# Optimization experiments

Measured on AMD Instinct MI355X. Metric: run time of the kernel, lower is better.

Reference implementation:

```python
import jax, jax.numpy as jnp
import numpy as np

B, C, H, W = 16, 256, 96, 96
CQ = C // 8      # 32, query/key channels in CrossAttention
CM = C // 2      # 128, inter_planes


def conv1x1(x, w, b=None):
    # x: [B,Cin,H,W], w: [Cout,Cin]
    y = jnp.einsum('bchw,oc->bohw', x, w)
    if b is not None:
        y = y + b[None, :, None, None]
    return y


def cross_attention(x, wq, bq, wk, bk, wv, bv, gamma):
    # criss-cross (axial H and W) attention with -inf diagonal on the H branch
    b_, c_, h_, w_ = x.shape
    q = conv1x1(x, wq, bq)  # [B,CQ,H,W]
    k = conv1x1(x, wk, bk)
    v = conv1x1(x, wv, bv)  # [B,C,H,W]
    # energy over column (H axis): [B,H,W,H], masked diag h==h'
    e_h = jnp.einsum('bchw,bckw->bhwk', q, k)
    diag = jnp.eye(h_, dtype=bool)[None, :, None, :]  # [1,H,1,H]
    e_h = jnp.where(diag, -jnp.inf, e_h)
    # energy over row (W axis): [B,H,W,W]
    e_w = jnp.einsum('bchw,bchv->bhwv', q, k)
    att = jax.nn.softmax(jnp.concatenate([e_h, e_w], axis=3), axis=3)
    a_h, a_w = att[..., :h_], att[..., h_:]
    out_h = jnp.einsum('bckw,bhwk->bchw', v, a_h)
    out_w = jnp.einsum('bchv,bhwv->bchw', v, a_w)
    return gamma * (out_h + out_w) + x


def spatial_weighted(x, w_q_right, w_v_right, w_up, b_up):
    b_, _, h_, w_ = x.shape
    inp = conv1x1(x, w_v_right).reshape(b_, CM, h_ * w_)        # [B,CM,HW]
    mask = conv1x1(x, w_q_right).reshape(b_, 1, h_ * w_)        # [B,1,HW]
    mask = jax.nn.softmax(mask, axis=2)
    ctx = jnp.einsum('bcn,bon->bco', inp, mask)                 # [B,CM,1]
    ctx = jnp.einsum('bci,oc->boi', ctx, w_up) + b_up[None, :, None]  # [B,C,1]
    mask_ch = jax.nn.sigmoid(ctx)[..., None]                    # [B,C,1,1]
    return x * mask_ch


def channel_weighted(x, w_q_left, w_v_left):
    b_, _, h_, w_ = x.shape
    g = conv1x1(x, w_q_left)                                    # [B,CM,H,W]
    avg = jnp.mean(g, axis=(2, 3))                              # [B,CM]
    theta = conv1x1(x, w_v_left).reshape(b_, CM, h_ * w_)       # [B,CM,HW]
    ctx = jnp.einsum('bc,bcn->bn', avg, theta)                  # [B,HW]
    ctx = jax.nn.softmax(ctx, axis=1).reshape(b_, 1, h_, w_)
    return x * jax.nn.sigmoid(ctx)


def setup_inputs() -> dict:
    key = jax.random.key(0)
    ks = jax.random.split(key, 16)
    s = lambda fan_in: (2.0 / fan_in) ** 0.5
    inp = {
        'x': jax.random.normal(ks[0], (B, C, H, W), jnp.float32),
        'w_q_right': jax.random.normal(ks[1], (1, C), jnp.float32) * s(C),
        'w_v_right': jax.random.normal(ks[2], (CM, C), jnp.float32) * s(C),
        'w_up': jax.random.normal(ks[3], (C, CM), jnp.float32) * s(CM),
        'b_up': jnp.zeros((C,), jnp.float32),
        'w_q_left': jax.random.normal(ks[4], (CM, C), jnp.float32) * s(C),
        'w_v_left': jax.random.normal(ks[5], (CM, C), jnp.float32) * s(C),
        'cr_wq': jax.random.normal(ks[6], (CQ, C), jnp.float32) * s(C),
        'cr_bq': jnp.zeros((CQ,), jnp.float32),
        'cr_wk': jax.random.normal(ks[7], (CQ, C), jnp.float32) * s(C),
        'cr_bk': jnp.zeros((CQ,), jnp.float32),
        'cr_wv': jax.random.normal(ks[8], (C, C), jnp.float32) * s(C),
        'cr_bv': jnp.zeros((C,), jnp.float32),
        'gamma': jax.random.normal(ks[9], (1,), jnp.float32) * 0.1,
    }
    return inp


def reference(x, w_q_right, w_v_right, w_up, b_up, w_q_left, w_v_left,
              cr_wq, cr_bq, cr_wk, cr_bk, cr_wv, cr_bv, gamma):
    cross = lambda t: cross_attention(t, cr_wq, cr_bq, cr_wk, cr_bk, cr_wv, cr_bv, gamma)
    ctx_channel = cross(spatial_weighted(x, w_q_right, w_v_right, w_up, b_up))
    ctx_spatial = cross(channel_weighted(x, w_q_left, w_v_left))
    return cross(ctx_spatial + ctx_channel)
```

## Files before the change

### kernel.cpp

```cpp
#include <hip/hip_runtime.h>
#include <math.h>

#define Bn 16
#define Cn 256
#define Hn 96
#define Wn 96
#define Nn 9216
#define PIXn 147456
#define XSZk ((size_t)Bn*Cn*Nn)
#define YSZk ((size_t)Bn*64*Nn)
#define ATTSZ ((size_t)PIXn*96)

typedef short bf8 __attribute__((ext_vector_type(8)));
typedef float f32x4 __attribute__((ext_vector_type(4)));
#define MFMA(a,b,c) __builtin_amdgcn_mfma_f32_16x16x32_bf16(a,b,c,0,0,0)

typedef unsigned short ushort_t;
typedef _Float16 h16;

__device__ inline ushort_t f2bf(float f){
  union{float f; unsigned int u;} v; v.f=f;
  unsigned int r = v.u + 0x7fffu + ((v.u>>16)&1u);
  return (ushort_t)(r>>16);
}
__device__ inline float bf2f(ushort_t s){
  union{unsigned int u; float f;} v; v.u = ((unsigned int)s)<<16;
  return v.f;
}
__device__ inline ushort_t f2h(float f){
  union{h16 h; ushort_t u;} v; v.h=(h16)f; return v.u;
}
__device__ inline float h2f(ushort_t u){
  union{ushort_t u; h16 h;} v; v.u=u; return (float)v.h;
}

__device__ inline float waveSum(float v){
#pragma unroll
  for(int o=32;o;o>>=1) v += __shfl_down(v,o,64);
  return v;
}
__device__ inline float waveMax(float v){
#pragma unroll
  for(int o=32;o;o>>=1) v = fmaxf(v,__shfl_down(v,o,64));
  return v;
}


__global__ __launch_bounds__(1024) void k_pass1(const float* __restrict__ x,
    const float* __restrict__ wqr, float* __restrict__ xmean,
    float* __restrict__ partp){
  int cg = blockIdx.x, b = blockIdx.y, tid = threadIdx.x;
  __shared__ float r16[16];
  float mp[9];
#pragma unroll
  for(int k=0;k<9;k++) mp[k]=0.f;
  for(int cc=0;cc<16;cc++){
    int c = cg*16+cc;
    const float* row = x + ((size_t)b*Cn + c)*Nn;
    float w = wqr[c];
    float s = 0.f;
#pragma unroll
    for(int k=0;k<9;k++){
      float v = row[k*1024+tid];
      s += v;
      mp[k] += w*v;
    }
    s = waveSum(s);
    if((tid&63)==0) r16[tid>>6]=s;
    __syncthreads();
    if(tid==0){
      float t=0.f;
      for(int i=0;i<16;i++) t+=r16[i];
      xmean[(size_t)b*Cn + c] = t*(1.f/Nn);
    }
    __syncthreads();
  }
  float* dst = partp + ((size_t)cg*Bn + b)*Nn;
#pragma unroll
  for(int k=0;k<9;k++) dst[k*1024+tid]=mp[k];
}

__global__ __launch_bounds__(1024) void k_pass2(const float* __restrict__ x,
    const float* __restrict__ wvec, const float* __restrict__ maskb,
    float* __restrict__ xw, float* __restrict__ partp){
  int cg = blockIdx.x, b = blockIdx.y, tid = threadIdx.x;
  __shared__ float r16[16];
  float cp[9], mk[9];
#pragma unroll
  for(int k=0;k<9;k++){
    cp[k]=0.f;
    mk[k]=maskb[(size_t)b*Nn + k*1024+tid];
  }
  for(int cc=0;cc<16;cc++){
    int c = cg*16+cc;
    const float* row = x + ((size_t)b*Cn + c)*Nn;
    float w = wvec[(size_t)b*Cn + c];
    float s = 0.f;
#pragma unroll
    for(int k=0;k<9;k++){
      float v = row[k*1024+tid];
      s += mk[k]*v;
      cp[k] += w*v;
    }
    s = waveSum(s);
    if((tid&63)==0) r16[tid>>6]=s;
    __syncthreads();
    if(tid==0){
      float t=0.f;
      for(int i=0;i<16;i++) t+=r16[i];
      xw[(size_t)b*Cn + c] = t;
    }
    __syncthreads();
  }
  float* dst = partp + ((size_t)cg*Bn + b)*Nn;
#pragma unroll
  for(int k=0;k<9;k++) dst[k*1024+tid]=cp[k];
}

__global__ void k_red16(const float* __restrict__ part, float* __restrict__ out){
  size_t p = (size_t)blockIdx.x*256 + threadIdx.x;
  float s=0.f;
#pragma unroll
  for(int cg=0;cg<16;cg++) s += part[(size_t)cg*Bn*Nn + p];
  out[p]=s;
}

__global__ void k_small1(const float* __restrict__ xmean, const float* __restrict__ wql,
                         const float* __restrict__ wvl, float* __restrict__ wvec){
  int b=blockIdx.x, t=threadIdx.x;
  __shared__ float xm[Cn];
  __shared__ float av[128];
  xm[t] = xmean[b*Cn+t];
  __syncthreads();
  if(t<128){
    float s=0.f;
    for(int c=0;c<Cn;c++) s += wql[t*Cn+c]*xm[c];
    av[t]=s;
  }
  __syncthreads();
  float s=0.f;
  for(int m=0;m<128;m++) s += av[m]*wvl[m*Cn+t];
  wvec[b*Cn+t]=s;
}

__global__ void k_softmax_n(const float* __restrict__ in, float* __restrict__ out, int mode){
  int b=blockIdx.x, tid=threadIdx.x, lane=tid&63, wid=tid>>6;
  const float* p = in + (size_t)b*Nn;
  __shared__ float red[16];
  __shared__ float bc2[2];
  float mx=-3e38f;
  for(int i=tid;i<Nn;i+=1024) mx=fmaxf(mx,p[i]);
  mx = waveMax(mx);
  if(lane==0) red[wid]=mx;
  __syncthreads();
  if(tid==0){ float m=red[0]; for(int i=1;i<16;i++) m=fmaxf(m,red[i]); bc2[0]=m; }
  __syncthreads();
  mx=bc2[0];
  float s=0.f;
  for(int i=tid;i<Nn;i+=1024) s+=expf(p[i]-mx);
  s = waveSum(s);
  __syncthreads();
  if(lane==0) red[wid]=s;
  __syncthreads();
  if(tid==0){ float t=0.f; for(int i=0;i<16;i++) t+=red[i]; bc2[1]=t; }
  __syncthreads();
  float inv=1.f/bc2[1];
  for(int i=tid;i<Nn;i+=1024){
    float e=expf(p[i]-mx)*inv;
    out[(size_t)b*Nn+i] = mode ? 1.f/(1.f+expf(-e)) : e;
  }
}

__global__ void k_small2(const float* __restrict__ xw, const float* __restrict__ wvr,
                         const float* __restrict__ wup, const float* __restrict__ bup,
                         float* __restrict__ g1){
  int b=blockIdx.x, t=threadIdx.x;
  __shared__ float xs[Cn];
  __shared__ float cx[128];
  xs[t]=xw[b*Cn+t];
  __syncthreads();
  if(t<128){
    float s=0.f;
    for(int c=0;c<Cn;c++) s += wvr[t*Cn+c]*xs[c];
    cx[t]=s;
  }
  __syncthreads();
  float s=bup[t];
  for(int m=0;m<128;m++) s += wup[t*128+m]*cx[m];
  g1[b*Cn+t]=1.f/(1.f+expf(-s));
}


__global__ void k_packb(const float* __restrict__ wq, const float* __restrict__ bq,
                        const float* __restrict__ wk, const float* __restrict__ bk,
                        const float* __restrict__ wv, const float* __restrict__ bv,
                        ushort_t* __restrict__ Wp, float* __restrict__ bp){
  int o = blockIdx.x, t = threadIdx.x;
  const float* src; float bs;
  if(o<32){ src = wq + o*Cn; bs = bq[o]; }
  else if(o<64){ src = wk + (o-32)*Cn; bs = bk[o-32]; }
  else { src = wv + (o-64)*Cn; bs = bv[o-64]; }
  Wp[o*Cn+t] = f2bf(src[t]);
  if(t==0) bp[o] = bs;
}

#define AP 40
#define BP 264
#define GP 68

template<int GATED>
__global__ __launch_bounds__(256) void k_gemm_qkv(
    const ushort_t* __restrict__ tb, const float* __restrict__ x,
    const float* __restrict__ g1, const float* __restrict__ m2,
    const ushort_t* __restrict__ Wp, const float* __restrict__ bp,
    ushort_t* __restrict__ Yqk, ushort_t* __restrict__ Vb, int selbase){
  __shared__ ushort_t SM[320*AP + 64*BP];
  __shared__ float gsh[256];
  ushort_t* Ws = SM;
  ushort_t* Bt = SM + 320*AP;
  int by = blockIdx.y, b = by & 15, sl = by >> 4;
  int sel = selbase + sl;
  int n0 = blockIdx.x*64;
  int tid = threadIdx.x, lane = tid&63, wid = tid>>6;

  if(GATED){
    gsh[tid] = g1[b*Cn + tid];
    __syncthreads();
    const float* xb = x + (size_t)b*Cn*Nn + n0 + (tid&63);
    float scl_n = (sel==1) ? m2[(size_t)b*Nn + n0 + (tid&63)] : 0.f;
    int cg = (tid>>6)*8;
#pragma unroll
    for(int p=0;p<8;p++){
      int c8 = p*32 + cg;
      float fv[8];
#pragma unroll
      for(int k2=0;k2<8;k2++){
        float xf = xb[(size_t)(c8+k2)*Nn];
        fv[k2] = xf * (sel==0 ? gsh[c8+k2] : scl_n);
      }
      uint4 pk;
      pk.x = (unsigned)f2bf(fv[0]) | ((unsigned)f2bf(fv[1])<<16);
      pk.y = (unsigned)f2bf(fv[2]) | ((unsigned)f2bf(fv[3])<<16);
      pk.z = (unsigned)f2bf(fv[4]) | ((unsigned)f2bf(fv[5])<<16);
      pk.w = (unsigned)f2bf(fv[6]) | ((unsigned)f2bf(fv[7])<<16);
      *(uint4*)&Bt[(tid&63)*BP + c8] = pk;
    }
  } else {
    const ushort_t* xb = tb + (size_t)b*Cn*Nn + n0 + (tid&63);
    int cg = (tid>>6)*8;
#pragma unroll
    for(int p=0;p<8;p++){
      int c8 = p*32 + cg;
      unsigned e0=xb[(size_t)(c8+0)*Nn], e1=xb[(size_t)(c8+1)*Nn];
      unsigned e2=xb[(size_t)(c8+2)*Nn], e3=xb[(size_t)(c8+3)*Nn];
      unsigned e4=xb[(size_t)(c8+4)*Nn], e5=xb[(size_t)(c8+5)*Nn];
      unsigned e6=xb[(size_t)(c8+6)*Nn], e7=xb[(size_t)(c8+7)*Nn];
      uint4 pk;
      pk.x = e0 | (e1<<16); pk.y = e2 | (e3<<16);
      pk.z = e4 | (e5<<16); pk.w = e6 | (e7<<16);
      *(uint4*)&Bt[(tid&63)*BP + c8] = pk;
    }
  }

  f32x4 acc[5][4];
#pragma unroll
  for(int f=0;f<5;f++)
#pragma unroll
    for(int g=0;g<4;g++) acc[f][g] = (f32x4){0.f,0.f,0.f,0.f};

  for(int ki=0;ki<8;ki++){
    __syncthreads();
#pragma unroll
    for(int q=0;q<5;q++){
      int fidx = q*256 + tid;
      int o = fidx>>2, kk = (fidx&3)*8;
      uint4 wv = *(const uint4*)&Wp[o*Cn + ki*32 + kk];
      *(uint4*)&Ws[o*AP + kk] = wv;
    }
    __syncthreads();
    bf8 bfr[4];
#pragma unroll
    for(int g=0;g<4;g++)
      bfr[g] = *(const bf8*)&Bt[(g*16 + (lane&15))*BP + ki*32 + (lane>>4)*8];
#pragma unroll
    for(int f=0;f<5;f++){
      bf8 a = *(const bf8*)&Ws[(wid*80 + f*16 + (lane&15))*AP + (lane>>4)*8];
#pragma unroll
      for(int g=0;g<4;g++) acc[f][g] = MFMA(a, bfr[g], acc[f][g]);
    }
  }

  __syncthreads();
#pragma unroll
  for(int f=0;f<5;f++){
    int o = wid*80 + f*16 + (lane>>4)*4;
#pragma unroll
    for(int i=0;i<4;i++){
      float bias = bp[o+i];
#pragma unroll
      for(int g=0;g<4;g++)
        SM[(o+i)*GP + g*16 + (lane&15)] = f2bf(acc[f][g][i] + bias);
    }
  }
  __syncthreads();
  ushort_t* Yo = Yqk + (size_t)sl*YSZk;
  ushort_t* Vo = Vb  + (size_t)sl*XSZk;
  for(int u=tid; u<320*8; u+=256){
    int lo_ = u>>3, c8 = (u&7)*8;
    ushort_t* dst = (lo_<64) ? (Yo + ((size_t)b*64 + lo_)*Nn)
                             : (Vo + ((size_t)b*Cn + (lo_-64))*Nn);
    *(uint4*)&dst[n0 + c8] = *(uint4*)&SM[lo_*GP + c8];
  }
}

__global__ __launch_bounds__(256) void k_transpose_b(const ushort_t* __restrict__ src,
                                                     ushort_t* __restrict__ dst){
  __shared__ ushort_t Ls[96*98];
  size_t base = (size_t)blockIdx.x * Nn;
  int tid = threadIdx.x;
  for(int e=tid*2; e<Nn; e+=512){
    unsigned int u = *(const unsigned int*)&src[base+e];
    int r=e/96, c=e%96;
    *(unsigned int*)&Ls[r*98+c] = u;
  }
  __syncthreads();
  for(int e=tid*2; e<Nn; e+=512){
    int r=e/96, c=e%96;
    unsigned int u = (unsigned int)Ls[c*98+r] | (((unsigned int)Ls[(c+1)*98+r])<<16);
    *(unsigned int*)&dst[base+e] = u;
  }
}

__global__ __launch_bounds__(256) void k_e2(const ushort_t* __restrict__ Yqk,
    const ushort_t* __restrict__ Yqkt, ushort_t* __restrict__ attl,
    ushort_t* __restrict__ attr){
  __shared__ ushort_t Qt[96*AP];
  __shared__ ushort_t Kt[96*AP];
  int r = blockIdx.x, mode = blockIdx.y;
  int zz = blockIdx.z, b = zz & 15, sl = zz >> 4;
  const ushort_t* Y = (mode ? Yqk : Yqkt) + (size_t)sl*YSZk;
  int pm   = mode ? 1  : 96;
  int pr   = mode ? 96 : 1;
  ushort_t* attx = (mode ? attr : attl) + (size_t)sl*ATTSZ;
  int tid = threadIdx.x, lane = tid&63, wid = tid>>6;
  {
    int half = tid>>7;
    int cg   = (tid>>5)&3;
    int l32  = tid&31;
    ushort_t* T = half ? Kt : Qt;
    const ushort_t* S = Y + ((size_t)b*64 + half*32 + cg*8)*Nn + (size_t)r*96;
#pragma unroll
    for(int p=0;p<3;p++){
      int sp = p*32 + l32;
      unsigned e0=S[(size_t)0*Nn+sp], e1=S[(size_t)1*Nn+sp];
      unsigned e2=S[(size_t)2*Nn+sp], e3=S[(size_t)3*Nn+sp];
      unsigned e4=S[(size_t)4*Nn+sp], e5=S[(size_t)5*Nn+sp];
      unsigned e6=S[(size_t)6*Nn+sp], e7=S[(size_t)7*Nn+sp];
      uint4 pk;
      pk.x = e0 | (e1<<16); pk.y = e2 | (e3<<16);
      pk.z = e4 | (e5<<16); pk.w = e6 | (e7<<16);
      *(uint4*)&T[sp*AP + cg*8] = pk;
    }
  }
  __syncthreads();
  int mb = (wid>>1)*48, nb = (wid&1)*48;
  const f32x4 z4 = {0.f,0.f,0.f,0.f};
  f32x4 acc[3][3];
  bf8 a[3], bb[3];
#pragma unroll
  for(int f=0;f<3;f++) a[f] = *(const bf8*)&Qt[(mb+f*16+(lane&15))*AP + (lane>>4)*8];
#pragma unroll
  for(int g=0;g<3;g++) bb[g] = *(const bf8*)&Kt[(nb+g*16+(lane&15))*AP + (lane>>4)*8];
#pragma unroll
  for(int f=0;f<3;f++)
#pragma unroll
    for(int g=0;g<3;g++) acc[f][g] = MFMA(a[f], bb[g], z4);
#pragma unroll
  for(int f=0;f<3;f++)
#pragma unroll
    for(int i=0;i<4;i++){
      int m = mb + f*16 + (lane>>4)*4 + i;
      ushort_t* arow = attx + ((size_t)b*Nn + (size_t)m*pm + (size_t)r*pr)*96;
#pragma unroll
      for(int g=0;g<3;g++){
        int n = nb + g*16 + (lane&15);
        arow[n] = f2h(acc[f][g][i]);
      }
    }
}

__global__ __launch_bounds__(256) void k_softmax_ip(ushort_t* attl, ushort_t* attr){
  int wave = threadIdx.x>>6, l = threadIdx.x&63;
  int t = blockIdx.x*4 + wave;
  int zz = blockIdx.z, b = zz & 15, sl = zz >> 4;
  attl += (size_t)sl*ATTSZ; attr += (size_t)sl*ATTSZ;
  int i=0, base=0;
  while(base + (96-i) <= t){ base += 96-i; i++; }
  int j = i + (t-base);
  int hf = l>>5, l32 = l&31;
  int h = hf ? j : i, w = hf ? i : j;
  size_t p = (size_t)b*Nn + (size_t)h*96 + w;
  const ushort_t* al = attl + p*96;
  const ushort_t* ar = attr + p*96;
  float v[6];
#pragma unroll
  for(int k=0;k<3;k++){
    int el = l32 + 32*k;
    float vv = h2f(al[el]);
    v[k] = (el==h) ? -1e30f : vv;
  }
#pragma unroll
  for(int k=0;k<3;k++) v[3+k] = h2f(ar[l32 + 32*k]);
  float mx = v[0];
#pragma unroll
  for(int k=1;k<6;k++) mx = fmaxf(mx, v[k]);
#pragma unroll
  for(int o=16;o;o>>=1) mx = fmaxf(mx, __shfl_xor(mx, o, 64));
  float e[6], s=0.f;
#pragma unroll
  for(int k=0;k<6;k++){ e[k]=expf(v[k]-mx); s+=e[k]; }
#pragma unroll
  for(int o=16;o;o>>=1) s += __shfl_xor(s, o, 64);
  float inv = 1.f/s;
  size_t q = (size_t)b*Nn + (size_t)w*96 + h;
  ushort_t* oh = attl + q*96;
  ushort_t* ow = attr + p*96;
#pragma unroll
  for(int k=0;k<3;k++) oh[l32+32*k] = f2bf(e[k]*inv);
#pragma unroll
  for(int k=0;k<3;k++) ow[l32+32*k] = f2bf(e[3+k]*inv);
}

#define SP 120
#define RP 100

template<int FIN>
__global__ __launch_bounds__(256) void k_pv2(const ushort_t* __restrict__ VB,
    const ushort_t* __restrict__ VTb, const ushort_t* __restrict__ attw,
    const ushort_t* __restrict__ atth, const float* __restrict__ x,
    const float* __restrict__ g1, const float* __restrict__ m2,
    const ushort_t* __restrict__ residb, ushort_t* TT, float* __restrict__ Of,
    ushort_t* OTb, const float* __restrict__ gp, int selbase){
  __shared__ ushort_t SMEM[128*RP];
  int r = blockIdx.x, mode = blockIdx.y>>1, half = blockIdx.y&1;
  int zz = blockIdx.z, b = zz & 15, sl = zz >> 4;
  int sel = selbase + sl;
  float gm = gp[0];
  int tid = threadIdx.x, lane = tid&63, wid = tid>>6;
  const ushort_t* V = (mode ? VTb : VB) + (size_t)sl*XSZk;
  size_t vbase = (size_t)b*Cn*Nn + (size_t)r*96;
  bf8 vf[6];
#pragma unroll
  for(int f=0;f<2;f++)
#pragma unroll
    for(int j=0;j<3;j++)
      vf[f*3+j] = *(const bf8*)&V[vbase
        + (size_t)(half*128 + wid*32 + f*16 + (lane&15))*Nn + j*32 + (lane>>4)*8];
  const ushort_t* ab = (mode ? atth : attw) + (size_t)sl*ATTSZ
                     + ((size_t)b*Nn + (size_t)r*96)*96;
  for(int u=tid; u<96*12; u+=256){
    int n=u/12, j8=(u%12)*8;
    uint4 q = *(const uint4*)&ab[n*96 + j8];
    *(uint4*)&SMEM[n*SP + j8] = q;
  }
  __syncthreads();
  f32x4 acc[2][6];
#pragma unroll
  for(int f=0;f<2;f++)
#pragma unroll
    for(int g=0;g<6;g++) acc[f][g] = (f32x4){0.f,0.f,0.f,0.f};
#pragma unroll
  for(int j0=0;j0<3;j0++){
    bf8 bfr[6];
#pragma unroll
    for(int g=0;g<6;g++)
      bfr[g] = *(const bf8*)&SMEM[(g*16+(lane&15))*SP + j0*32 + (lane>>4)*8];
#pragma unroll
    for(int f=0;f<2;f++)
#pragma unroll
      for(int g=0;g<6;g++) acc[f][g] = MFMA(vf[f*3+j0], bfr[g], acc[f][g]);
  }
  __syncthreads();
#pragma unroll
  for(int f=0;f<2;f++){
    int lr = wid*32 + f*16 + (lane>>4)*4;
#pragma unroll
    for(int i=0;i<4;i++)
#pragma unroll
      for(int g=0;g<6;g++)
        SMEM[(lr+i)*RP + g*16 + (lane&15)] = f2bf(gm*acc[f][g][i]);
  }
  __syncthreads();
  ushort_t* OT = OTb + (size_t)sl*XSZk;
  ushort_t* To = TT + (size_t)sel*XSZk;
  for(int u=tid; u<128*12; u+=256){
    int lc = u/12, q8 = (u%12)*8;
    int c = half*128 + lc;
    size_t row = vbase + (size_t)c*Nn;
    uint4 v = *(uint4*)&SMEM[lc*RP + q8];
    if(mode){
      *(uint4*)&OT[row + q8] = v;
    } else {
      unsigned* vp=(unsigned*)&v;
      if(FIN){
        uint4 rv = *(const uint4*)&residb[row + q8];
        unsigned* rp=(unsigned*)&rv;
        float4 o1, o2;
        o1.x = bf2f((ushort_t)(vp[0]&0xffff)) + bf2f((ushort_t)(rp[0]&0xffff));
        o1.y = bf2f((ushort_t)(vp[0]>>16))    + bf2f((ushort_t)(rp[0]>>16));
        o1.z = bf2f((ushort_t)(vp[1]&0xffff)) + bf2f((ushort_t)(rp[1]&0xffff));
        o1.w = bf2f((ushort_t)(vp[1]>>16))    + bf2f((ushort_t)(rp[1]>>16));
        o2.x = bf2f((ushort_t)(vp[2]&0xffff)) + bf2f((ushort_t)(rp[2]&0xffff));
        o2.y = bf2f((ushort_t)(vp[2]>>16))    + bf2f((ushort_t)(rp[2]>>16));
        o2.z = bf2f((ushort_t)(vp[3]&0xffff)) + bf2f((ushort_t)(rp[3]&0xffff));
        o2.w = bf2f((ushort_t)(vp[3]>>16))    + bf2f((ushort_t)(rp[3]>>16));
        *(float4*)&Of[row + q8]     = o1;
        *(float4*)&Of[row + q8 + 4] = o2;
      } else {
        float4 x1 = *(const float4*)&x[row + q8];
        float4 x2 = *(const float4*)&x[row + q8 + 4];
        float rs[8];
        if(sel==0){
          float g = g1[b*Cn + c];
          rs[0]=x1.x*g; rs[1]=x1.y*g; rs[2]=x1.z*g; rs[3]=x1.w*g;
          rs[4]=x2.x*g; rs[5]=x2.y*g; rs[6]=x2.z*g; rs[7]=x2.w*g;
        } else {
          float4 m1 = *(const float4*)&m2[(size_t)b*Nn + (size_t)r*96 + q8];
          float4 m2v= *(const float4*)&m2[(size_t)b*Nn + (size_t)r*96 + q8 + 4];
          rs[0]=x1.x*m1.x; rs[1]=x1.y*m1.y; rs[2]=x1.z*m1.z; rs[3]=x1.w*m1.w;
          rs[4]=x2.x*m2v.x; rs[5]=x2.y*m2v.y; rs[6]=x2.z*m2v.z; rs[7]=x2.w*m2v.w;
        }
        uint4 o; unsigned* op=(unsigned*)&o;
#pragma unroll
        for(int k=0;k<4;k++){
          float lo = bf2f((ushort_t)(vp[k]&0xffff)) + rs[2*k];
          float hi = bf2f((ushort_t)(vp[k]>>16))    + rs[2*k+1];
          op[k] = (unsigned)f2bf(lo) | ((unsigned)f2bf(hi)<<16);
        }
        *(uint4*)&To[row + q8] = o;
      }
    }
  }
}

template<int VAR>
__global__ __launch_bounds__(256) void k_merge(float* __restrict__ outf,
    ushort_t* __restrict__ outb, const ushort_t* __restrict__ add,
    const ushort_t* __restrict__ OT){
  __shared__ ushort_t Ls[96*98];
  __shared__ ushort_t Ls2[(VAR==3)?96*98:1];
  size_t base = (size_t)blockIdx.x * Nn;
  int tid = threadIdx.x;
  for(int e=tid*2; e<Nn; e+=512){
    int r=e/96, c=e%96;
    *(unsigned int*)&Ls[r*98+c] = *(const unsigned int*)&OT[base+e];
    if(VAR==3)
      *(unsigned int*)&Ls2[r*98+c] = *(const unsigned int*)&OT[XSZk + base + e];
  }
  __syncthreads();
  for(int e=tid*4; e<Nn; e+=1024){
    int r=e/96, c=e%96;
    float t0 = bf2f(Ls[(c+0)*98+r]), t1 = bf2f(Ls[(c+1)*98+r]);
    float t2 = bf2f(Ls[(c+2)*98+r]), t3 = bf2f(Ls[(c+3)*98+r]);
    if(VAR==3){
      t0 += bf2f(Ls2[(c+0)*98+r]); t1 += bf2f(Ls2[(c+1)*98+r]);
      t2 += bf2f(Ls2[(c+2)*98+r]); t3 += bf2f(Ls2[(c+3)*98+r]);
    }
    if(VAR==1){
      float4 o = *(float4*)&outf[base+e];
      o.x += t0; o.y += t1; o.z += t2; o.w += t3;
      *(float4*)&outf[base+e] = o;
    } else {
      uint2 u = *(uint2*)&outb[base+e];
      float a0 = bf2f((ushort_t)(u.x&0xffff)) + t0;
      float a1 = bf2f((ushort_t)(u.x>>16))    + t1;
      float a2 = bf2f((ushort_t)(u.y&0xffff)) + t2;
      float a3 = bf2f((ushort_t)(u.y>>16))    + t3;
      if(VAR==2 || VAR==3){
        uint2 v = *(const uint2*)&add[base+e];
        a0 += bf2f((ushort_t)(v.x&0xffff));
        a1 += bf2f((ushort_t)(v.x>>16));
        a2 += bf2f((ushort_t)(v.y&0xffff));
        a3 += bf2f((ushort_t)(v.y>>16));
      }
      u.x = (unsigned)f2bf(a0) | ((unsigned)f2bf(a1)<<16);
      u.y = (unsigned)f2bf(a2) | ((unsigned)f2bf(a3)<<16);
      *(uint2*)&outb[base+e] = u;
    }
  }
}

extern "C" void kernel_launch(void* const* d_in, const int* in_sizes, int n_in,
                              void* d_out, int out_size, void* d_ws, size_t ws_size,
                              hipStream_t stream){
  const float* x    = (const float*)d_in[0];
  const float* wqr  = (const float*)d_in[1];
  const float* wvr  = (const float*)d_in[2];
  const float* wup  = (const float*)d_in[3];
  const float* bup  = (const float*)d_in[4];
  const float* wql  = (const float*)d_in[5];
  const float* wvl  = (const float*)d_in[6];
  const float* crwq = (const float*)d_in[7];
  const float* crbq = (const float*)d_in[8];
  const float* crwk = (const float*)d_in[9];
  const float* crbk = (const float*)d_in[10];
  const float* crwv = (const float*)d_in[11];
  const float* crbv = (const float*)d_in[12];
  const float* gma  = (const float*)d_in[13];
  float* out = (float*)d_out;

  const int nsel = (ws_size >= (size_t)654000000) ? 2 : 1;

  char* wsb = (char*)d_ws;
  ushort_t* TT   = (ushort_t*)wsb; wsb += 2*XSZk*2;
  ushort_t* VB2  = (ushort_t*)wsb; wsb += (size_t)nsel*XSZk*2;
  ushort_t* VT2  = (ushort_t*)wsb; wsb += (size_t)nsel*XSZk*2;
  ushort_t* Y2   = (ushort_t*)wsb; wsb += (size_t)nsel*YSZk*2;
  ushort_t* Yt2  = (ushort_t*)wsb; wsb += (size_t)nsel*YSZk*2;
  ushort_t* ATTL = (ushort_t*)wsb; wsb += (size_t)nsel*ATTSZ*2;
  ushort_t* ATTR = (ushort_t*)wsb; wsb += (size_t)nsel*ATTSZ*2;
  float*    partp= (float*)wsb;    wsb += (size_t)16*Bn*Nn*4;
  ushort_t* Wpb  = (ushort_t*)wsb; wsb += 320*Cn*2;
  float*    bp   = (float*)wsb;    wsb += 320*4;
  float*    xmean= (float*)wsb;    wsb += Bn*Cn*4;
  float*    wvec = (float*)wsb;    wsb += Bn*Cn*4;
  float*    xw   = (float*)wsb;    wsb += Bn*Cn*4;
  float*    g1   = (float*)wsb;    wsb += Bn*Cn*4;
  float*    mraw = (float*)wsb;    wsb += (size_t)PIXn*4;
  float*    maskb= (float*)wsb;    wsb += (size_t)PIXn*4;
  float*    craw = (float*)wsb;    wsb += (size_t)PIXn*4;
  float*    m2   = (float*)wsb;    wsb += (size_t)PIXn*4;

  k_packb<<<320,256,0,stream>>>(crwq,crbq,crwk,crbk,crwv,crbv,Wpb,bp);

  k_pass1<<<dim3(16,Bn),1024,0,stream>>>(x, wqr, xmean, partp);
  k_red16<<<Bn*Nn/256,256,0,stream>>>(partp, mraw);
  k_small1<<<Bn,256,0,stream>>>(xmean, wql, wvl, wvec);
  k_softmax_n<<<Bn,1024,0,stream>>>(mraw, maskb, 0);
  k_pass2<<<dim3(16,Bn),1024,0,stream>>>(x, wvec, maskb, xw, partp);
  k_red16<<<Bn*Nn/256,256,0,stream>>>(partp, craw);
  k_softmax_n<<<Bn,1024,0,stream>>>(craw, m2, 1);
  k_small2<<<Bn,256,0,stream>>>(xw, wvr, wup, bup, g1);

  auto cross12 = [&](int selbase, int nsl){
    k_gemm_qkv<1><<<dim3(Nn/64,Bn*nsl),256,0,stream>>>(nullptr, x, g1, m2, Wpb, bp, Y2, VB2, selbase);
    k_transpose_b<<<Bn*64*nsl,256,0,stream>>>(Y2, Yt2);
    k_e2<<<dim3(96,2,Bn*nsl),256,0,stream>>>(Y2, Yt2, ATTL, ATTR);
    k_softmax_ip<<<dim3(1164,1,Bn*nsl),256,0,stream>>>(ATTL, ATTR);
    k_transpose_b<<<Bn*Cn*nsl,256,0,stream>>>(VB2, VT2);
    k_pv2<0><<<dim3(96,4,Bn*nsl),256,0,stream>>>(VB2, VT2, ATTR, ATTL,
        x, g1, m2, nullptr, TT, nullptr, VT2, gma, selbase);
  };

  ushort_t* T2p = TT + XSZk;
  if(nsel==2){
    cross12(0, 2);
    k_merge<3><<<Bn*Cn,256,0,stream>>>(nullptr, TT, T2p, VT2);
  } else {
    cross12(0, 1);
    k_merge<0><<<Bn*Cn,256,0,stream>>>(nullptr, TT, nullptr, VT2);
    cross12(1, 1);
    k_merge<2><<<Bn*Cn,256,0,stream>>>(nullptr, TT, T2p, VT2);
  }

  k_gemm_qkv<0><<<dim3(Nn/64,Bn),256,0,stream>>>(TT, nullptr, nullptr, nullptr, Wpb, bp, Y2, VB2, 0);
  k_transpose_b<<<Bn*64,256,0,stream>>>(Y2, Yt2);
  k_e2<<<dim3(96,2,Bn),256,0,stream>>>(Y2, Yt2, ATTL, ATTR);
  k_softmax_ip<<<dim3(1164,1,Bn),256,0,stream>>>(ATTL, ATTR);
  k_transpose_b<<<Bn*Cn,256,0,stream>>>(VB2, VT2);
  k_pv2<1><<<dim3(96,4,Bn),256,0,stream>>>(VB2, VT2, ATTR, ATTL,
      nullptr, nullptr, nullptr, TT, nullptr, out, VT2, gma, 0);
  k_merge<1><<<Bn*Cn,256,0,stream>>>(out, nullptr, nullptr, VT2);
}
```

Measured before the change: 1.145 ms.

## Cache bf16 copy of x, vectorize reductions, drop batched dual-branch path

The first reduction pass now also writes a bf16 copy of x into the workspace. Later passes (pass2, the gated QKV GEMM and the PV residual) read this half-size copy instead of fp32 x when the workspace is large enough. The pass kernels switch to float4-vectorized contiguous chunks of 8 pixels per thread. The two-slice batched cross-attention path is removed in favour of always running the branches sequentially. The final PV now writes a bf16 intermediate that a new merge variant adds into the fp32 output. This cuts fp32 read traffic but adds extra rounding of x and loses the batched-branch concurrency.

```diff
diff --git a/kernel.cpp b/kernel.cpp
--- a/kernel.cpp
+++ b/kernel.cpp
@@ -46,24 +46,41 @@
 }
 
 
+template<int XBW>
 __global__ __launch_bounds__(1024) void k_pass1(const float* __restrict__ x,
     const float* __restrict__ wqr, float* __restrict__ xmean,
-    float* __restrict__ partp){
+    float* __restrict__ partp, ushort_t* __restrict__ XB){
   int cg = blockIdx.x, b = blockIdx.y, tid = threadIdx.x;
   __shared__ float r16[16];
-  float mp[9];
-#pragma unroll
-  for(int k=0;k<9;k++) mp[k]=0.f;
+  float mp[2][8];
+#pragma unroll
+  for(int u=0;u<2;u++)
+#pragma unroll
+    for(int e=0;e<8;e++) mp[u][e]=0.f;
   for(int cc=0;cc<16;cc++){
     int c = cg*16+cc;
     const float* row = x + ((size_t)b*Cn + c)*Nn;
     float w = wqr[c];
     float s = 0.f;
 #pragma unroll
-    for(int k=0;k<9;k++){
-      float v = row[k*1024+tid];
-      s += v;
-      mp[k] += w*v;
+    for(int u=0;u<2;u++){
+      int ch = tid + u*1024;
+      if(ch < 1152){
+        float4 a = *(const float4*)&row[ch*8];
+        float4 d = *(const float4*)&row[ch*8+4];
+        float v0=a.x,v1=a.y,v2=a.z,v3=a.w,v4=d.x,v5=d.y,v6=d.z,v7=d.w;
+        s += ((v0+v1)+(v2+v3))+((v4+v5)+(v6+v7));
+        mp[u][0]+=w*v0; mp[u][1]+=w*v1; mp[u][2]+=w*v2; mp[u][3]+=w*v3;
+        mp[u][4]+=w*v4; mp[u][5]+=w*v5; mp[u][6]+=w*v6; mp[u][7]+=w*v7;
+        if(XBW){
+          uint4 pk;
+          pk.x=(unsigned)f2bf(v0)|((unsigned)f2bf(v1)<<16);
+          pk.y=(unsigned)f2bf(v2)|((unsigned)f2bf(v3)<<16);
+          pk.z=(unsigned)f2bf(v4)|((unsigned)f2bf(v5)<<16);
+          pk.w=(unsigned)f2bf(v6)|((unsigned)f2bf(v7)<<16);
+          *(uint4*)&XB[((size_t)b*Cn + c)*Nn + ch*8] = pk;
+        }
+      }
     }
     s = waveSum(s);
     if((tid&63)==0) r16[tid>>6]=s;
@@ -77,30 +94,68 @@
   }
   float* dst = partp + ((size_t)cg*Bn + b)*Nn;
 #pragma unroll
-  for(int k=0;k<9;k++) dst[k*1024+tid]=mp[k];
-}
-
+  for(int u=0;u<2;u++){
+    int ch = tid + u*1024;
+    if(ch < 1152){
+      float4 o1, o2;
+      o1.x=mp[u][0]; o1.y=mp[u][1]; o1.z=mp[u][2]; o1.w=mp[u][3];
+      o2.x=mp[u][4]; o2.y=mp[u][5]; o2.z=mp[u][6]; o2.w=mp[u][7];
+      *(float4*)&dst[ch*8]   = o1;
+      *(float4*)&dst[ch*8+4] = o2;
+    }
+  }
+}
+
+template<int XBR>
 __global__ __launch_bounds__(1024) void k_pass2(const float* __restrict__ x,
-    const float* __restrict__ wvec, const float* __restrict__ maskb,
-    float* __restrict__ xw, float* __restrict__ partp){
+    const ushort_t* __restrict__ XB, const float* __restrict__ wvec,
+    const float* __restrict__ maskb, float* __restrict__ xw,
+    float* __restrict__ partp){
   int cg = blockIdx.x, b = blockIdx.y, tid = threadIdx.x;
   __shared__ float r16[16];
-  float cp[9], mk[9];
-#pragma unroll
-  for(int k=0;k<9;k++){
-    cp[k]=0.f;
-    mk[k]=maskb[(size_t)b*Nn + k*1024+tid];
+  float cp[2][8], mk[2][8];
+#pragma unroll
+  for(int u=0;u<2;u++){
+    int ch = tid + u*1024;
+    if(ch < 1152){
+      float4 a = *(const float4*)&maskb[(size_t)b*Nn + ch*8];
+      float4 d = *(const float4*)&maskb[(size_t)b*Nn + ch*8 + 4];
+      mk[u][0]=a.x; mk[u][1]=a.y; mk[u][2]=a.z; mk[u][3]=a.w;
+      mk[u][4]=d.x; mk[u][5]=d.y; mk[u][6]=d.z; mk[u][7]=d.w;
+    }
+#pragma unroll
+    for(int e=0;e<8;e++) cp[u][e]=0.f;
   }
   for(int cc=0;cc<16;cc++){
     int c = cg*16+cc;
-    const float* row = x + ((size_t)b*Cn + c)*Nn;
     float w = wvec[(size_t)b*Cn + c];
     float s = 0.f;
 #pragma unroll
-    for(int k=0;k<9;k++){
-      float v = row[k*1024+tid];
-      s += mk[k]*v;
-      cp[k] += w*v;
+    for(int u=0;u<2;u++){
+      int ch = tid + u*1024;
+      if(ch < 1152){
+        float v[8];
+        if(XBR){
+          uint4 q = *(const uint4*)&XB[((size_t)b*Cn + c)*Nn + ch*8];
+          unsigned* qp=(unsigned*)&q;
+#pragma unroll
+          for(int k=0;k<4;k++){
+            v[2*k]   = bf2f((ushort_t)(qp[k]&0xffff));
+            v[2*k+1] = bf2f((ushort_t)(qp[k]>>16));
+          }
+        } else {
+          const float* row = x + ((size_t)b*Cn + c)*Nn;
+          float4 a = *(const float4*)&row[ch*8];
+          float4 d = *(const float4*)&row[ch*8+4];
+          v[0]=a.x; v[1]=a.y; v[2]=a.z; v[3]=a.w;
+          v[4]=d.x; v[5]=d.y; v[6]=d.z; v[7]=d.w;
+        }
+#pragma unroll
+        for(int e=0;e<8;e++){
+          s += mk[u][e]*v[e];
+          cp[u][e] += w*v[e];
+        }
+      }
     }
     s = waveSum(s);
     if((tid&63)==0) r16[tid>>6]=s;
@@ -114,7 +169,16 @@
   }
   float* dst = partp + ((size_t)cg*Bn + b)*Nn;
 #pragma unroll
-  for(int k=0;k<9;k++) dst[k*1024+tid]=cp[k];
+  for(int u=0;u<2;u++){
+    int ch = tid + u*1024;
+    if(ch < 1152){
+      float4 o1, o2;
+      o1.x=cp[u][0]; o1.y=cp[u][1]; o1.z=cp[u][2]; o1.w=cp[u][3];
+      o2.x=cp[u][4]; o2.y=cp[u][5]; o2.z=cp[u][6]; o2.w=cp[u][7];
+      *(float4*)&dst[ch*8]   = o1;
+      *(float4*)&dst[ch*8+4] = o2;
+    }
+  }
 }
 
 __global__ void k_red16(const float* __restrict__ part, float* __restrict__ out){
@@ -208,35 +272,44 @@
 #define BP 264
 #define GP 68
 
-template<int GATED>
+template<int GATED, int XBR>
 __global__ __launch_bounds__(256) void k_gemm_qkv(
     const ushort_t* __restrict__ tb, const float* __restrict__ x,
+    const ushort_t* __restrict__ XBp,
     const float* __restrict__ g1, const float* __restrict__ m2,
     const ushort_t* __restrict__ Wp, const float* __restrict__ bp,
-    ushort_t* __restrict__ Yqk, ushort_t* __restrict__ Vb, int selbase){
+    ushort_t* __restrict__ Yqk, ushort_t* __restrict__ Vb, int sel){
   __shared__ ushort_t SM[320*AP + 64*BP];
   __shared__ float gsh[256];
   ushort_t* Ws = SM;
   ushort_t* Bt = SM + 320*AP;
-  int by = blockIdx.y, b = by & 15, sl = by >> 4;
-  int sel = selbase + sl;
+  int b = blockIdx.y;
   int n0 = blockIdx.x*64;
   int tid = threadIdx.x, lane = tid&63, wid = tid>>6;
 
   if(GATED){
     gsh[tid] = g1[b*Cn + tid];
     __syncthreads();
-    const float* xb = x + (size_t)b*Cn*Nn + n0 + (tid&63);
     float scl_n = (sel==1) ? m2[(size_t)b*Nn + n0 + (tid&63)] : 0.f;
     int cg = (tid>>6)*8;
 #pragma unroll
     for(int p=0;p<8;p++){
       int c8 = p*32 + cg;
       float fv[8];
-#pragma unroll
-      for(int k2=0;k2<8;k2++){
-        float xf = xb[(size_t)(c8+k2)*Nn];
-        fv[k2] = xf * (sel==0 ? gsh[c8+k2] : scl_n);
+      if(XBR){
+        const ushort_t* xb = XBp + (size_t)b*Cn*Nn + n0 + (tid&63);
+#pragma unroll
+        for(int k2=0;k2<8;k2++){
+          float xf = bf2f(xb[(size_t)(c8+k2)*Nn]);
+          fv[k2] = xf * (sel==0 ? gsh[c8+k2] : scl_n);
+        }
+      } else {
+        const float* xb = x + (size_t)b*Cn*Nn + n0 + (tid&63);
+#pragma unroll
+        for(int k2=0;k2<8;k2++){
+          float xf = xb[(size_t)(c8+k2)*Nn];
+          fv[k2] = xf * (sel==0 ? gsh[c8+k2] : scl_n);
+        }
       }
       uint4 pk;
       pk.x = (unsigned)f2bf(fv[0]) | ((unsigned)f2bf(fv[1])<<16);
@@ -303,12 +376,10 @@
     }
   }
   __syncthreads();
-  ushort_t* Yo = Yqk + (size_t)sl*YSZk;
-  ushort_t* Vo = Vb  + (size_t)sl*XSZk;
   for(int u=tid; u<320*8; u+=256){
     int lo_ = u>>3, c8 = (u&7)*8;
-    ushort_t* dst = (lo_<64) ? (Yo + ((size_t)b*64 + lo_)*Nn)
-                             : (Vo + ((size_t)b*Cn + (lo_-64))*Nn);
+    ushort_t* dst = (lo_<64) ? (Yqk + ((size_t)b*64 + lo_)*Nn)
+                             : (Vb + ((size_t)b*Cn + (lo_-64))*Nn);
     *(uint4*)&dst[n0 + c8] = *(uint4*)&SM[lo_*GP + c8];
   }
 }
@@ -336,12 +407,11 @@
     ushort_t* __restrict__ attr){
   __shared__ ushort_t Qt[96*AP];
   __shared__ ushort_t Kt[96*AP];
-  int r = blockIdx.x, mode = blockIdx.y;
-  int zz = blockIdx.z, b = zz & 15, sl = zz >> 4;
-  const ushort_t* Y = (mode ? Yqk : Yqkt) + (size_t)sl*YSZk;
+  int r = blockIdx.x, mode = blockIdx.y, b = blockIdx.z;
+  const ushort_t* Y = mode ? Yqk : Yqkt;
   int pm   = mode ? 1  : 96;
   int pr   = mode ? 96 : 1;
-  ushort_t* attx = (mode ? attr : attl) + (size_t)sl*ATTSZ;
+  ushort_t* attx = mode ? attr : attl;
   int tid = threadIdx.x, lane = tid&63, wid = tid>>6;
   {
     int half = tid>>7;
@@ -392,8 +462,7 @@
 __global__ __launch_bounds__(256) void k_softmax_ip(ushort_t* attl, ushort_t* attr){
   int wave = threadIdx.x>>6, l = threadIdx.x&63;
   int t = blockIdx.x*4 + wave;
-  int zz = blockIdx.z, b = zz & 15, sl = zz >> 4;
-  attl += (size_t)sl*ATTSZ; attr += (size_t)sl*ATTSZ;
+  int b = blockIdx.z;
   int i=0, base=0;
   while(base + (96-i) <= t){ base += 96-i; i++; }
   int j = i + (t-base);
@@ -434,20 +503,19 @@
 #define SP 120
 #define RP 100
 
-template<int FIN>
+template<int RES, int XBR>
 __global__ __launch_bounds__(256) void k_pv2(const ushort_t* __restrict__ VB,
     const ushort_t* __restrict__ VTb, const ushort_t* __restrict__ attw,
     const ushort_t* __restrict__ atth, const float* __restrict__ x,
+    const ushort_t* __restrict__ XBp,
     const float* __restrict__ g1, const float* __restrict__ m2,
-    const ushort_t* __restrict__ residb, ushort_t* TT, float* __restrict__ Of,
-    ushort_t* OTb, const float* __restrict__ gp, int selbase){
+    const ushort_t* __restrict__ residb, ushort_t* __restrict__ Tob,
+    ushort_t* __restrict__ OTb, const float* __restrict__ gp, int sel){
   __shared__ ushort_t SMEM[128*RP];
-  int r = blockIdx.x, mode = blockIdx.y>>1, half = blockIdx.y&1;
-  int zz = blockIdx.z, b = zz & 15, sl = zz >> 4;
-  int sel = selbase + sl;
+  int r = blockIdx.x, mode = blockIdx.y>>1, half = blockIdx.y&1, b = blockIdx.z;
   float gm = gp[0];
   int tid = threadIdx.x, lane = tid&63, wid = tid>>6;
-  const ushort_t* V = (mode ? VTb : VB) + (size_t)sl*XSZk;
+  const ushort_t* V = mode ? VTb : VB;
   size_t vbase = (size_t)b*Cn*Nn + (size_t)r*96;
   bf8 vf[6];
 #pragma unroll
@@ -456,8 +524,7 @@
     for(int j=0;j<3;j++)
       vf[f*3+j] = *(const bf8*)&V[vbase
         + (size_t)(half*128 + wid*32 + f*16 + (lane&15))*Nn + j*32 + (lane>>4)*8];
-  const ushort_t* ab = (mode ? atth : attw) + (size_t)sl*ATTSZ
-                     + ((size_t)b*Nn + (size_t)r*96)*96;
+  const ushort_t* ab = (mode ? atth : attw) + ((size_t)b*Nn + (size_t)r*96)*96;
   for(int u=tid; u<96*12; u+=256){
     int n=u/12, j8=(u%12)*8;
     uint4 q = *(const uint4*)&ab[n*96 + j8];
@@ -491,54 +558,60 @@
         SMEM[(lr+i)*RP + g*16 + (lane&15)] = f2bf(gm*acc[f][g][i]);
   }
   __syncthreads();
-  ushort_t* OT = OTb + (size_t)sl*XSZk;
-  ushort_t* To = TT + (size_t)sel*XSZk;
   for(int u=tid; u<128*12; u+=256){
     int lc = u/12, q8 = (u%12)*8;
     int c = half*128 + lc;
     size_t row = vbase + (size_t)c*Nn;
     uint4 v = *(uint4*)&SMEM[lc*RP + q8];
     if(mode){
-      *(uint4*)&OT[row + q8] = v;
+      *(uint4*)&OTb[row + q8] = v;
     } else {
       unsigned* vp=(unsigned*)&v;
-      if(FIN){
+      float rs[8];
+      if(RES==1){
         uint4 rv = *(const uint4*)&residb[row + q8];
         unsigned* rp=(unsigned*)&rv;
-        float4 o1, o2;
-        o1.x = bf2f((ushort_t)(vp[0]&0xffff)) + bf2f((ushort_t)(rp[0]&0xffff));
-        o1.y = bf2f((ushort_t)(vp[0]>>16))    + bf2f((ushort_t)(rp[0]>>16));
-        o1.z = bf2f((ushort_t)(vp[1]&0xffff)) + bf2f((ushort_t)(rp[1]&0xffff));
-        o1.w = bf2f((ushort_t)(vp[1]>>16))    + bf2f((ushort_t)(rp[1]>>16));
-        o2.x = bf2f((ushort_t)(vp[2]&0xffff)) + bf2f((ushort_t)(rp[2]&0xffff));
-        o2.y = bf2f((ushort_t)(vp[2]>>16))    + bf2f((ushort_t)(rp[2]>>16));
-        o2.z = bf2f((ushort_t)(vp[3]&0xffff)) + bf2f((ushort_t)(rp[3]&0xffff));
-        o2.w = bf2f((ushort_t)(vp[3]>>16))    + bf2f((ushort_t)(rp[3]>>16));
-        *(float4*)&Of[row + q8]     = o1;
-        *(float4*)&Of[row + q8 + 4] = o2;
+#pragma unroll
+        for(int k=0;k<4;k++){
+          rs[2*k]   = bf2f((ushort_t)(rp[k]&0xffff));
+          rs[2*k+1] = bf2f((ushort_t)(rp[k]>>16));
+        }
       } else {
-        float4 x1 = *(const float4*)&x[row + q8];
-        float4 x2 = *(const float4*)&x[row + q8 + 4];
-        float rs[8];
+        float xv[8];
+        if(XBR){
+          uint4 xq = *(const uint4*)&XBp[row + q8];
+          unsigned* xp=(unsigned*)&xq;
+#pragma unroll
+          for(int k=0;k<4;k++){
+            xv[2*k]   = bf2f((ushort_t)(xp[k]&0xffff));
+            xv[2*k+1] = bf2f((ushort_t)(xp[k]>>16));
+          }
+        } else {
+          float4 x1 = *(const float4*)&x[row + q8];
+          float4 x2 = *(const float4*)&x[row + q8 + 4];
+          xv[0]=x1.x; xv[1]=x1.y; xv[2]=x1.z; xv[3]=x1.w;
+          xv[4]=x2.x; xv[5]=x2.y; xv[6]=x2.z; xv[7]=x2.w;
+        }
         if(sel==0){
           float g = g1[b*Cn + c];
-          rs[0]=x1.x*g; rs[1]=x1.y*g; rs[2]=x1.z*g; rs[3]=x1.w*g;
-          rs[4]=x2.x*g; rs[5]=x2.y*g; rs[6]=x2.z*g; rs[7]=x2.w*g;
+#pragma unroll
+          for(int k=0;k<8;k++) rs[k] = xv[k]*g;
         } else {
           float4 m1 = *(const float4*)&m2[(size_t)b*Nn + (size_t)r*96 + q8];
           float4 m2v= *(const float4*)&m2[(size_t)b*Nn + (size_t)r*96 + q8 + 4];
-          rs[0]=x1.x*m1.x; rs[1]=x1.y*m1.y; rs[2]=x1.z*m1.z; rs[3]=x1.w*m1.w;
-          rs[4]=x2.x*m2v.x; rs[5]=x2.y*m2v.y; rs[6]=x2.z*m2v.z; rs[7]=x2.w*m2v.w;
+          float mv[8] = {m1.x,m1.y,m1.z,m1.w,m2v.x,m2v.y,m2v.z,m2v.w};
+#pragma unroll
+          for(int k=0;k<8;k++) rs[k] = xv[k]*mv[k];
         }
-        uint4 o; unsigned* op=(unsigned*)&o;
-#pragma unroll
-        for(int k=0;k<4;k++){
-          float lo = bf2f((ushort_t)(vp[k]&0xffff)) + rs[2*k];
-          float hi = bf2f((ushort_t)(vp[k]>>16))    + rs[2*k+1];
-          op[k] = (unsigned)f2bf(lo) | ((unsigned)f2bf(hi)<<16);
-        }
-        *(uint4*)&To[row + q8] = o;
       }
+      uint4 o; unsigned* op=(unsigned*)&o;
+#pragma unroll
+      for(int k=0;k<4;k++){
+        float lo = bf2f((ushort_t)(vp[k]&0xffff)) + rs[2*k];
+        float hi = bf2f((ushort_t)(vp[k]>>16))    + rs[2*k+1];
+        op[k] = (unsigned)f2bf(lo) | ((unsigned)f2bf(hi)<<16);
+      }
+      *(uint4*)&Tob[row + q8] = o;
     }
   }
 }
@@ -548,27 +621,24 @@
     ushort_t* __restrict__ outb, const ushort_t* __restrict__ add,
     const ushort_t* __restrict__ OT){
   __shared__ ushort_t Ls[96*98];
-  __shared__ ushort_t Ls2[(VAR==3)?96*98:1];
   size_t base = (size_t)blockIdx.x * Nn;
   int tid = threadIdx.x;
   for(int e=tid*2; e<Nn; e+=512){
     int r=e/96, c=e%96;
     *(unsigned int*)&Ls[r*98+c] = *(const unsigned int*)&OT[base+e];
-    if(VAR==3)
-      *(unsigned int*)&Ls2[r*98+c] = *(const unsigned int*)&OT[XSZk + base + e];
   }
   __syncthreads();
   for(int e=tid*4; e<Nn; e+=1024){
     int r=e/96, c=e%96;
     float t0 = bf2f(Ls[(c+0)*98+r]), t1 = bf2f(Ls[(c+1)*98+r]);
     float t2 = bf2f(Ls[(c+2)*98+r]), t3 = bf2f(Ls[(c+3)*98+r]);
-    if(VAR==3){
-      t0 += bf2f(Ls2[(c+0)*98+r]); t1 += bf2f(Ls2[(c+1)*98+r]);
-      t2 += bf2f(Ls2[(c+2)*98+r]); t3 += bf2f(Ls2[(c+3)*98+r]);
-    }
-    if(VAR==1){
-      float4 o = *(float4*)&outf[base+e];
-      o.x += t0; o.y += t1; o.z += t2; o.w += t3;
+    if(VAR==4){
+      uint2 v = *(const uint2*)&add[base+e];
+      float4 o;
+      o.x = bf2f((ushort_t)(v.x&0xffff)) + t0;
+      o.y = bf2f((ushort_t)(v.x>>16))    + t1;
+      o.z = bf2f((ushort_t)(v.y&0xffff)) + t2;
+      o.w = bf2f((ushort_t)(v.y>>16))    + t3;
       *(float4*)&outf[base+e] = o;
     } else {
       uint2 u = *(uint2*)&outb[base+e];
@@ -576,7 +646,7 @@
       float a1 = bf2f((ushort_t)(u.x>>16))    + t1;
       float a2 = bf2f((ushort_t)(u.y&0xffff)) + t2;
       float a3 = bf2f((ushort_t)(u.y>>16))    + t3;
-      if(VAR==2 || VAR==3){
+      if(VAR==2){
         uint2 v = *(const uint2*)&add[base+e];
         a0 += bf2f((ushort_t)(v.x&0xffff));
         a1 += bf2f((ushort_t)(v.x>>16));
@@ -609,16 +679,14 @@
   const float* gma  = (const float*)d_in[13];
   float* out = (float*)d_out;
 
-  const int nsel = (ws_size >= (size_t)654000000) ? 2 : 1;
-
   char* wsb = (char*)d_ws;
   ushort_t* TT   = (ushort_t*)wsb; wsb += 2*XSZk*2;
-  ushort_t* VB2  = (ushort_t*)wsb; wsb += (size_t)nsel*XSZk*2;
-  ushort_t* VT2  = (ushort_t*)wsb; wsb += (size_t)nsel*XSZk*2;
-  ushort_t* Y2   = (ushort_t*)wsb; wsb += (size_t)nsel*YSZk*2;
-  ushort_t* Yt2  = (ushort_t*)wsb; wsb += (size_t)nsel*YSZk*2;
-  ushort_t* ATTL = (ushort_t*)wsb; wsb += (size_t)nsel*ATTSZ*2;
-  ushort_t* ATTR = (ushort_t*)wsb; wsb += (size_t)nsel*ATTSZ*2;
+  ushort_t* VB2  = (ushort_t*)wsb; wsb += XSZk*2;
+  ushort_t* VT2  = (ushort_t*)wsb; wsb += XSZk*2;
+  ushort_t* Y2   = (ushort_t*)wsb; wsb += YSZk*2;
+  ushort_t* Yt2  = (ushort_t*)wsb; wsb += YSZk*2;
+  ushort_t* ATTL = (ushort_t*)wsb; wsb += ATTSZ*2;
+  ushort_t* ATTR = (ushort_t*)wsb; wsb += ATTSZ*2;
   float*    partp= (float*)wsb;    wsb += (size_t)16*Bn*Nn*4;
   ushort_t* Wpb  = (ushort_t*)wsb; wsb += 320*Cn*2;
   float*    bp   = (float*)wsb;    wsb += 320*4;
@@ -630,45 +698,47 @@
   float*    maskb= (float*)wsb;    wsb += (size_t)PIXn*4;
   float*    craw = (float*)wsb;    wsb += (size_t)PIXn*4;
   float*    m2   = (float*)wsb;    wsb += (size_t)PIXn*4;
+  ushort_t* XB   = (ushort_t*)wsb;
+  const int useXB = (ws_size >= (size_t)484000000) ? 1 : 0;
 
   k_packb<<<320,256,0,stream>>>(crwq,crbq,crwk,crbk,crwv,crbv,Wpb,bp);
 
-  k_pass1<<<dim3(16,Bn),1024,0,stream>>>(x, wqr, xmean, partp);
+  if(useXB) k_pass1<1><<<dim3(16,Bn),1024,0,stream>>>(x, wqr, xmean, partp, XB);
+  else      k_pass1<0><<<dim3(16,Bn),1024,0,stream>>>(x, wqr, xmean, partp, nullptr);
   k_red16<<<Bn*Nn/256,256,0,stream>>>(partp, mraw);
   k_small1<<<Bn,256,0,stream>>>(xmean, wql, wvl, wvec);
   k_softmax_n<<<Bn,1024,0,stream>>>(mraw, maskb, 0);
-  k_pass2<<<dim3(16,Bn),1024,0,stream>>>(x, wvec, maskb, xw, partp);
+  if(useXB) k_pass2<1><<<dim3(16,Bn),1024,0,stream>>>(nullptr, XB, wvec, maskb, xw, partp);
+  else      k_pass2<0><<<dim3(16,Bn),1024,0,stream>>>(x, nullptr, wvec, maskb, xw, partp);
   k_red16<<<Bn*Nn/256,256,0,stream>>>(partp, craw);
   k_softmax_n<<<Bn,1024,0,stream>>>(craw, m2, 1);
   k_small2<<<Bn,256,0,stream>>>(xw, wvr, wup, bup, g1);
 
-  auto cross12 = [&](int selbase, int nsl){
-    k_gemm_qkv<1><<<dim3(Nn/64,Bn*nsl),256,0,stream>>>(nullptr, x, g1, m2, Wpb, bp, Y2, VB2, selbase);
-    k_transpose_b<<<Bn*64*nsl,256,0,stream>>>(Y2, Yt2);
-    k_e2<<<dim3(96,2,Bn*nsl),256,0,stream>>>(Y2, Yt2, ATTL, ATTR);
-    k_softmax_ip<<<dim3(1164,1,Bn*nsl),256,0,stream>>>(ATTL, ATTR);
-    k_transpose_b<<<Bn*Cn*nsl,256,0,stream>>>(VB2, VT2);
-    k_pv2<0><<<dim3(96,4,Bn*nsl),256,0,stream>>>(VB2, VT2, ATTR, ATTL,
-        x, g1, m2, nullptr, TT, nullptr, VT2, gma, selbase);
+  ushort_t* T2p = TT + XSZk;
+
+  auto crossg = [&](int sel){
+    if(useXB) k_gemm_qkv<1,1><<<dim3(Nn/64,Bn),256,0,stream>>>(nullptr, nullptr, XB, g1, m2, Wpb, bp, Y2, VB2, sel);
+    else      k_gemm_qkv<1,0><<<dim3(Nn/64,Bn),256,0,stream>>>(nullptr, x, nullptr, g1, m2, Wpb, bp, Y2, VB2, sel);
+    k_transpose_b<<<Bn*64,256,0,stream>>>(Y2, Yt2);
+    k_e2<<<dim3(96,2,Bn),256,0,stream>>>(Y2, Yt2, ATTL, ATTR);
+    k_softmax_ip<<<dim3(1164,1,Bn),256,0,stream>>>(ATTL, ATTR);
+    k_transpose_b<<<Bn*Cn,256,0,stream>>>(VB2, VT2);
+    ushort_t* To = TT + (size_t)sel*XSZk;
+    if(useXB) k_pv2<0,1><<<dim3(96,4,Bn),256,0,stream>>>(VB2, VT2, ATTR, ATTL, nullptr, XB, g1, m2, nullptr, To, VT2, gma, sel);
+    else      k_pv2<0,0><<<dim3(96,4,Bn),256,0,stream>>>(VB2, VT2, ATTR, ATTL, x, nullptr, g1, m2, nullptr, To, VT2, gma, sel);
   };
 
-  ushort_t* T2p = TT + XSZk;
-  if(nsel==2){
-    cross12(0, 2);
-    k_merge<3><<<Bn*Cn,256,0,stream>>>(nullptr, TT, T2p, VT2);
-  } else {
-    cross12(0, 1);
-    k_merge<0><<<Bn*Cn,256,0,stream>>>(nullptr, TT, nullptr, VT2);
-    cross12(1, 1);
-    k_merge<2><<<Bn*Cn,256,0,stream>>>(nullptr, TT, T2p, VT2);
-  }
-
-  k_gemm_qkv<0><<<dim3(Nn/64,Bn),256,0,stream>>>(TT, nullptr, nullptr, nullptr, Wpb, bp, Y2, VB2, 0);
+  crossg(0);
+  k_merge<0><<<Bn*Cn,256,0,stream>>>(nullptr, TT, nullptr, VT2);
+  crossg(1);
+  k_merge<2><<<Bn*Cn,256,0,stream>>>(nullptr, TT, T2p, VT2);
+
+  k_gemm_qkv<0,0><<<dim3(Nn/64,Bn),256,0,stream>>>(TT, nullptr, nullptr, nullptr, nullptr, Wpb, bp, Y2, VB2, 0);
   k_transpose_b<<<Bn*64,256,0,stream>>>(Y2, Yt2);
   k_e2<<<dim3(96,2,Bn),256,0,stream>>>(Y2, Yt2, ATTL, ATTR);
   k_softmax_ip<<<dim3(1164,1,Bn),256,0,stream>>>(ATTL, ATTR);
   k_transpose_b<<<Bn*Cn,256,0,stream>>>(VB2, VT2);
-  k_pv2<1><<<dim3(96,4,Bn),256,0,stream>>>(VB2, VT2, ATTR, ATTL,
-      nullptr, nullptr, nullptr, TT, nullptr, out, VT2, gma, 0);
-  k_merge<1><<<Bn*Cn,256,0,stream>>>(out, nullptr, nullptr, VT2);
-}
+  k_pv2<1,0><<<dim3(96,4,Bn),256,0,stream>>>(VB2, VT2, ATTR, ATTL,
+      nullptr, nullptr, nullptr, nullptr, TT, T2p, VT2, gma, 0);
+  k_merge<4><<<Bn*Cn,256,0,stream>>>(out, nullptr, T2p, VT2);
+}
```

After: 1.118 ms. -2.3%, faster.
